# Kernel tuning notes

Measured on AMD Instinct MI355X. Metric: run time of the kernel, lower is better.

Reference implementation:

```python
import jax, jax.numpy as jnp
import numpy as np

NU, NUS, NI, NIS = 50000, 20000, 100000, 20000
E_US, E_IS, E_UI = 200000, 400000, 500000
NUM_USERS, NUM_ITEMS, UCODE, ICODE = 500000, 1000000, 1024, 1024
D, H, FH, B = 64, 4, 32, 1024  # embed_size, num_heads, gnn_hidden_size, batch

# (name, src_in_dim, dst_in_dim, out_feats_per_head)
REL_SPECS = [("r1", D, D, FH),            # user -shares-> u_sem
             ("r2", D, D, FH),            # item -shares-> i_sem
             ("r3", H * FH + D, D, FH),   # i_sem -denotes-> item
             ("r4", H * FH + D, D, FH),   # u_sem -denotes-> user
             ("r5", H * FH, H * FH, D)]   # item -clicked_by-> user


def setup_inputs() -> dict:
    key = jax.random.key(0)
    ks = iter(jax.random.split(key, 64))
    nrm = lambda shape: jax.random.normal(next(ks), shape, jnp.float32) * 0.05
    ri = lambda shape, hi: jax.random.randint(next(ks), shape, 0, hi, jnp.int32)
    inp = {}
    # node ids / edge lists / output gather indices (replaces boolean mask)
    inp["user_ids"] = ri((NU,), NUM_USERS)
    inp["usem_ids"] = ri((NUS,), UCODE)
    inp["item_ids"] = ri((NI,), NUM_ITEMS)
    inp["isem_ids"] = ri((NIS,), ICODE)
    inp["us_src"], inp["us_dst"] = ri((E_US,), NU), ri((E_US,), NUS)
    inp["is_src"], inp["is_dst"] = ri((E_IS,), NI), ri((E_IS,), NIS)
    inp["ui_src"], inp["ui_dst"] = ri((E_UI,), NI), ri((E_UI,), NU)
    inp["user_out_idx"] = ri((B,), NU)
    # embedding tables (padding rows included for user/u_sem)
    inp["user_table"] = nrm((NUM_USERS + 1, D))
    inp["usem_table"] = nrm((UCODE + 1, D))
    inp["item_table"] = nrm((NUM_ITEMS, D))
    inp["isem_table"] = nrm((ICODE, D))
    # GATConv params per relation: fc_src, fc_dst (no bias), attn_l, attn_r, out bias
    for name, ds, dd, fo in REL_SPECS:
        inp[name + "_Wsrc"] = nrm((ds, H * fo))
        inp[name + "_Wdst"] = nrm((dd, H * fo))
        inp[name + "_al"] = nrm((H, fo))
        inp[name + "_ar"] = nrm((H, fo))
        inp[name + "_b"] = nrm((H * fo,))
    # user_gnn_mapping: Linear(embed_size*num_heads -> embed_size) + ReLU (dropout=eval identity)
    inp["Wm"] = nrm((D * H, D))
    inp["bm"] = nrm((D,))
    return inp


def gat(xs, xd, es, ed, Wsrc, Wdst, al, ar, b, fo):
    """DGL bipartite GATConv, allow_zero_in_degree=True, leaky_relu(0.2) attention."""
    nd = xd.shape[0]
    fs = (xs @ Wsrc).reshape(-1, H, fo)   # [Ns,H,F]
    fd = (xd @ Wdst).reshape(-1, H, fo)   # [Nd,H,F]
    el = jnp.einsum("nhf,hf->nh", fs, al)
    er = jnp.einsum("nhf,hf->nh", fd, ar)
    e = jax.nn.leaky_relu(el[es] + er[ed], 0.2)            # [E,H]
    m = jax.ops.segment_max(e, ed, num_segments=nd)
    m = jnp.where(jnp.isfinite(m), m, 0.0)                 # empty segments -> 0
    ex = jnp.exp(e - m[ed])
    den = jax.ops.segment_sum(ex, ed, num_segments=nd)
    alpha = ex / jnp.maximum(den[ed], 1e-12)               # edge softmax per dst
    out = jax.ops.segment_sum(alpha[:, :, None] * fs[es], ed, num_segments=nd)
    return out + b.reshape(1, H, fo)                       # [Nd,H,F]


def reference(user_table, usem_table, item_table, isem_table,
              r1_Wsrc, r1_Wdst, r1_al, r1_ar, r1_b,
              r2_Wsrc, r2_Wdst, r2_al, r2_ar, r2_b,
              r3_Wsrc, r3_Wdst, r3_al, r3_ar, r3_b,
              r4_Wsrc, r4_Wdst, r4_al, r4_ar, r4_b,
              r5_Wsrc, r5_Wdst, r5_al, r5_ar, r5_b,
              Wm, bm,
              user_ids, usem_ids, item_ids, isem_ids,
              us_src, us_dst, is_src, is_dst, ui_src, ui_dst, user_out_idx):
    user_emb = user_table[user_ids]            # [NU,D]
    u_quant = usem_table[usem_ids]             # [NUS,D]
    # user -shares-> u_sem
    u_n = gat(user_emb, u_quant, us_src, us_dst, r1_Wsrc, r1_Wdst, r1_al, r1_ar, r1_b, FH).reshape(NUS, H * FH)
    # u_sem -denotes-> user ('denotes' edges are reversed 'shares' edges)
    u_h = gat(jnp.concatenate([u_n, u_quant], -1), user_emb, us_dst, us_src,
              r4_Wsrc, r4_Wdst, r4_al, r4_ar, r4_b, FH).reshape(NU, H * FH)
    item_emb = item_table[item_ids]
    i_quant = isem_table[isem_ids]
    i_n = gat(item_emb, i_quant, is_src, is_dst, r2_Wsrc, r2_Wdst, r2_al, r2_ar, r2_b, FH).reshape(NIS, H * FH)
    i_h = gat(jnp.concatenate([i_n, i_quant], -1), item_emb, is_dst, is_src,
              r3_Wsrc, r3_Wdst, r3_al, r3_ar, r3_b, FH).reshape(NI, H * FH)
    # item -clicked_by-> user
    h = gat(i_h, u_h, ui_src, ui_dst, r5_Wsrc, r5_Wdst, r5_al, r5_ar, r5_b, D).reshape(NU, H * D)
    h = h[user_out_idx]                        # masked gather of batch users [B, H*D]
    return jax.nn.relu(h @ Wm + bm)            # user_gnn_mapping (dropout=eval)
```

## Files before the change

### kernel.cpp

```cpp
#include <hip/hip_runtime.h>
#include <math.h>

#define NU 50000
#define NUS 20000
#define NI 100000
#define NIS 20000
#define E_US 200000
#define E_IS 400000
#define E_UI 500000
#define BQ 1024
#define NT 240000
#define EPOOL (2 * E_US + 2 * E_IS + E_UI)

static __device__ __forceinline__ float4 f4zero() { return make_float4(0.f, 0.f, 0.f, 0.f); }

static __device__ __forceinline__ void fma4(float4& acc, float s, const float4& w) {
  acc.x = fmaf(s, w.x, acc.x);
  acc.y = fmaf(s, w.y, acc.y);
  acc.z = fmaf(s, w.z, acc.z);
  acc.w = fmaf(s, w.w, acc.w);
}

__global__ void gather_all(const float* __restrict__ t0, const int* __restrict__ id0,
                           float* __restrict__ o0, int n0, const float* __restrict__ t1,
                           const int* __restrict__ id1, float* __restrict__ o1, int n1,
                           const float* __restrict__ t2, const int* __restrict__ id2,
                           float* __restrict__ o2, int n2, const float* __restrict__ t3,
                           const int* __restrict__ id3, float* __restrict__ o3, int n3) {
  int y = blockIdx.y;
  const float* t;
  const int* id;
  float* o;
  int n;
  if (y == 0) { t = t0; id = id0; o = o0; n = n0; }
  else if (y == 1) { t = t1; id = id1; o = o1; n = n1; }
  else if (y == 2) { t = t2; id = id2; o = o2; n = n2; }
  else { t = t3; id = id3; o = o3; n = n3; }
  int i = blockIdx.x * blockDim.x + threadIdx.x;
  if (i >= n * 16) return;
  int row = i >> 4, j = i & 15;
  ((float4*)o)[i] = ((const float4*)(t + (size_t)id[row] * 64))[j];
}

struct EdgeSets {
  const int* es[5];
  const int* ed[5];
  int E[5];
  int base[5];
};

__global__ void zero_ints(int* __restrict__ p, int n) {
  int i = blockIdx.x * blockDim.x + threadIdx.x;
  if (i < n) p[i] = 0;
}

__global__ void hist5(EdgeSets S, int* __restrict__ cnt) {
  int y = blockIdx.y;
  int e = blockIdx.x * blockDim.x + threadIdx.x;
  if (e < S.E[y]) atomicAdd(&cnt[S.base[y] + S.ed[y][e]], 1);
}

__global__ void alloc_offsets(const int* __restrict__ cnt, int* __restrict__ start,
                              int* __restrict__ wo, int* __restrict__ cursor, int n) {
  int i = blockIdx.x * blockDim.x + threadIdx.x;
  int lane = threadIdx.x & 63;
  int c = (i < n) ? cnt[i] : 0;
  int s = c;
#pragma unroll
  for (int o = 1; o < 64; o <<= 1) {
    int y = __shfl_up(s, o);
    if (lane >= o) s += y;
  }
  int base = 0;
  if (lane == 63) base = atomicAdd(cursor, s);
  base = __shfl(base, 63);
  if (i < n) {
    int st = base + s - c;
    start[i] = st;
    wo[i] = st;
  }
}

__global__ void scatter5(EdgeSets S, int* __restrict__ wo, int* __restrict__ srcp) {
  int y = blockIdx.y;
  int e = blockIdx.x * blockDim.x + threadIdx.x;
  if (e < S.E[y]) {
    int p = atomicAdd(&wo[S.base[y] + S.ed[y][e]], 1);
    srcp[p] = S.es[y][e];
  }
}

__global__ __launch_bounds__(256, 2) void gemm_fused(
    const float* __restrict__ A1, int K1, const float* __restrict__ A2, int K2,
    const float* __restrict__ W, int Kout, const float* __restrict__ avec,
    float* __restrict__ logits, int fo_shift, float* __restrict__ C, int N) {
  __shared__ float Wlds[32 * 128];
  __shared__ float Alds[32 * 36];
  const int t = threadIdx.x;
  const int cbase = blockIdx.y * 128;
  const int colpos = t & 31;
  const int c0 = colpos << 2;
  const int rg = (t >> 5) << 2;
  const int sr = t >> 3;
  const int sk = (t & 7) << 2;
  const int rt = blockIdx.x * 32;
  const int KT = K1 + K2;

  float4 acc[4] = {f4zero(), f4zero(), f4zero(), f4zero()};
  for (int kc = 0; kc < KT; kc += 32) {
    __syncthreads();
    for (int i = t; i < 1024; i += 256) {
      int k = i >> 5, c4 = (i & 31) << 2;
      *(float4*)&Wlds[k * 128 + c4] = *(const float4*)&W[(size_t)(kc + k) * Kout + cbase + c4];
    }
    {
      int row = rt + sr;
      float4 v = f4zero();
      if (row < N) {
        if (kc < K1) v = *(const float4*)&A1[(size_t)row * K1 + kc + sk];
        else v = *(const float4*)&A2[(size_t)row * K2 + (kc - K1) + sk];
      }
      Alds[(sk + 0) * 36 + sr] = v.x;
      Alds[(sk + 1) * 36 + sr] = v.y;
      Alds[(sk + 2) * 36 + sr] = v.z;
      Alds[(sk + 3) * 36 + sr] = v.w;
    }
    __syncthreads();
#pragma unroll
    for (int k = 0; k < 32; ++k) {
      float4 w = *(float4*)&Wlds[k * 128 + c0];
      float4 a = *(float4*)&Alds[k * 36 + rg];
      fma4(acc[0], a.x, w);
      fma4(acc[1], a.y, w);
      fma4(acc[2], a.z, w);
      fma4(acc[3], a.w, w);
    }
  }
  if (C) {
#pragma unroll
    for (int ri = 0; ri < 4; ++ri) {
      int row = rt + rg + ri;
      if (row < N) *(float4*)&C[(size_t)row * Kout + cbase + c0] = acc[ri];
    }
  }
  if (avec) {
    float4 av = *(const float4*)&avec[cbase + c0];
    const int gsz = 1 << (fo_shift - 2);
    const int h = (cbase + c0) >> fo_shift;
    float part[4];
#pragma unroll
    for (int ri = 0; ri < 4; ++ri)
      part[ri] = acc[ri].x * av.x + acc[ri].y * av.y + acc[ri].z * av.z + acc[ri].w * av.w;
    for (int off = 1; off < gsz; off <<= 1) {
#pragma unroll
      for (int ri = 0; ri < 4; ++ri) part[ri] += __shfl_xor(part[ri], off);
    }
    if ((colpos & (gsz - 1)) == 0) {
#pragma unroll
      for (int ri = 0; ri < 4; ++ri) {
        int row = rt + rg + ri;
        if (row < N) logits[(size_t)row * 4 + h] = part[ri];
      }
    }
  }
}

template <int NF>
__global__ __launch_bounds__(256) void gat_aggregate(
    const float* __restrict__ fs, const float* __restrict__ el, const float* __restrict__ er,
    const int* __restrict__ srcp, const int* __restrict__ start, const int* __restrict__ cnt,
    const float* __restrict__ bias, float* __restrict__ out, int Nd, int nodeBase) {
  int node = (blockIdx.x * 256 + threadIdx.x) >> 6;
  if (node >= Nd) return;
  int lane = threadIdx.x & 63;
  constexpr int K = NF * 64;
  int h = lane >> 4;
  int f0 = lane * NF;
  float acc[NF] = {};
  float den = 0.f;
  float erh = er[(size_t)node * 4 + h];
  int s = start[nodeBase + node];
  int e1 = s + cnt[nodeBase + node];
  for (int p = s; p < e1; ++p) {
    int src = srcp[p];
    float z = el[(size_t)src * 4 + h] + erh;
    float x = expf(z > 0.f ? z : 0.2f * z);
    const float* fr = fs + (size_t)src * K + f0;
    if (NF == 2) {
      float2 v = *(const float2*)fr;
      acc[0] = fmaf(x, v.x, acc[0]);
      acc[1] = fmaf(x, v.y, acc[1]);
    } else {
      float4 v = *(const float4*)fr;
      acc[0] = fmaf(x, v.x, acc[0]);
      acc[1] = fmaf(x, v.y, acc[1]);
      acc[2] = fmaf(x, v.z, acc[2]);
      acc[3] = fmaf(x, v.w, acc[3]);
    }
    den += x;
  }
  float inv = 1.f / fmaxf(den, 1e-12f);
#pragma unroll
  for (int j = 0; j < NF; ++j)
    out[(size_t)node * K + f0 + j] = fmaf(acc[j], inv, bias[f0 + j]);
}

__global__ void final_mlp(const float* __restrict__ h5, const int* __restrict__ idx,
                          const float* __restrict__ Wm, const float* __restrict__ bm,
                          float* __restrict__ out, int Bn) {
  int wave = (blockIdx.x * 256 + threadIdx.x) >> 6;
  int lane = threadIdx.x & 63;
  if (wave >= Bn) return;
  const float* row = h5 + (size_t)idx[wave] * 256;
  float acc = bm[lane];
  for (int k = 0; k < 256; ++k) acc = fmaf(row[k], Wm[k * 64 + lane], acc);
  out[wave * 64 + lane] = fmaxf(acc, 0.f);
}

static inline int cdiv(int a, int b) { return (a + b - 1) / b; }

extern "C" void kernel_launch(void* const* d_in, const int* in_sizes, int n_in, void* d_out,
                              int out_size, void* d_ws, size_t ws_size, hipStream_t stream) {
  const int* user_ids = (const int*)d_in[0];
  const int* usem_ids = (const int*)d_in[1];
  const int* item_ids = (const int*)d_in[2];
  const int* isem_ids = (const int*)d_in[3];
  const int* us_src = (const int*)d_in[4];
  const int* us_dst = (const int*)d_in[5];
  const int* is_src = (const int*)d_in[6];
  const int* is_dst = (const int*)d_in[7];
  const int* ui_src = (const int*)d_in[8];
  const int* ui_dst = (const int*)d_in[9];
  const int* user_out_idx = (const int*)d_in[10];
  const float* user_table = (const float*)d_in[11];
  const float* usem_table = (const float*)d_in[12];
  const float* item_table = (const float*)d_in[13];
  const float* isem_table = (const float*)d_in[14];
  const float* R[5][5];
  for (int r = 0; r < 5; ++r)
    for (int j = 0; j < 5; ++j) R[r][j] = (const float*)d_in[15 + r * 5 + j];
  const float* Wm = (const float*)d_in[40];
  const float* bm = (const float*)d_in[41];
  float* out = (float*)d_out;

  float* ws = (float*)d_ws;
  size_t off = 0;
  auto alloc = [&](size_t n) {
    float* p = ws + off;
    off += (n + 3) & ~(size_t)3;
    return p;
  };
  float* user_emb = alloc((size_t)NU * 64);
  float* u_quant = alloc((size_t)NUS * 64);
  float* item_emb = alloc((size_t)NI * 64);
  float* i_quant = alloc((size_t)NIS * 64);
  float* u_n = alloc((size_t)NUS * 128);
  float* u_h = alloc((size_t)NU * 128);
  float* i_n = alloc((size_t)NIS * 128);
  float* i_h = alloc((size_t)NI * 128);
  float* h5 = alloc((size_t)NU * 256);
  float* fsb = alloc((size_t)NI * 256);
  float* elb = alloc((size_t)NI * 4);
  float* erb = alloc((size_t)NI * 4);
  int* cnt = (int*)alloc(NT + 4);
  int* startb = (int*)alloc(NT + 4);
  int* wob = (int*)alloc(NT + 4);
  int* srcp = (int*)alloc(EPOOL);

  EdgeSets S;
  S.es[0] = us_src; S.ed[0] = us_dst; S.E[0] = E_US; S.base[0] = 0;
  S.es[1] = us_dst; S.ed[1] = us_src; S.E[1] = E_US; S.base[1] = NUS;
  S.es[2] = is_src; S.ed[2] = is_dst; S.E[2] = E_IS; S.base[2] = NUS + NU;
  S.es[3] = is_dst; S.ed[3] = is_src; S.E[3] = E_IS; S.base[3] = NUS + NU + NIS;
  S.es[4] = ui_src; S.ed[4] = ui_dst; S.E[4] = E_UI; S.base[4] = NUS + NU + NIS + NI;

  zero_ints<<<cdiv(NT + 1, 1024), 1024, 0, stream>>>(cnt, NT + 1);
  gather_all<<<dim3(cdiv(NI * 16, 256), 4), 256, 0, stream>>>(
      user_table, user_ids, user_emb, NU, usem_table, usem_ids, u_quant, NUS, item_table,
      item_ids, item_emb, NI, isem_table, isem_ids, i_quant, NIS);
  hist5<<<dim3(cdiv(E_UI, 256), 5), 256, 0, stream>>>(S, cnt);
  alloc_offsets<<<cdiv(NT, 256), 256, 0, stream>>>(cnt, startb, wob, cnt + NT, NT);
  scatter5<<<dim3(cdiv(E_UI, 256), 5), 256, 0, stream>>>(S, wob, srcp);

  auto gemm = [&](const float* A1, int K1, const float* A2, int K2, const float* W, int Kout,
                  const float* av, float* lg, int fo_shift, float* Cc, int N) {
    gemm_fused<<<dim3(cdiv(N, 32), Kout / 128), 256, 0, stream>>>(A1, K1, A2, K2, W, Kout, av,
                                                                  lg, fo_shift, Cc, N);
  };
  auto agg = [&](int Kout, float* outb, const float* bias, int Nd, int base) {
    if (Kout == 128)
      gat_aggregate<2><<<cdiv(Nd, 4), 256, 0, stream>>>(fsb, elb, erb, srcp, startb, cnt, bias,
                                                        outb, Nd, base);
    else
      gat_aggregate<4><<<cdiv(Nd, 4), 256, 0, stream>>>(fsb, elb, erb, srcp, startb, cnt, bias,
                                                        outb, Nd, base);
  };

  gemm(user_emb, 64, nullptr, 0, R[0][0], 128, R[0][2], elb, 5, fsb, NU);
  gemm(u_quant, 64, nullptr, 0, R[0][1], 128, R[0][3], erb, 5, nullptr, NUS);
  agg(128, u_n, R[0][4], NUS, 0);
  gemm(u_n, 128, u_quant, 64, R[3][0], 128, R[3][2], elb, 5, fsb, NUS);
  gemm(user_emb, 64, nullptr, 0, R[3][1], 128, R[3][3], erb, 5, nullptr, NU);
  agg(128, u_h, R[3][4], NU, NUS);
  gemm(item_emb, 64, nullptr, 0, R[1][0], 128, R[1][2], elb, 5, fsb, NI);
  gemm(i_quant, 64, nullptr, 0, R[1][1], 128, R[1][3], erb, 5, nullptr, NIS);
  agg(128, i_n, R[1][4], NIS, NUS + NU);
  gemm(i_n, 128, i_quant, 64, R[2][0], 128, R[2][2], elb, 5, fsb, NIS);
  gemm(item_emb, 64, nullptr, 0, R[2][1], 128, R[2][3], erb, 5, nullptr, NI);
  agg(128, i_h, R[2][4], NI, NUS + NU + NIS);
  gemm(i_h, 128, nullptr, 0, R[4][0], 256, R[4][2], elb, 6, fsb, NI);
  gemm(u_h, 128, nullptr, 0, R[4][1], 256, R[4][3], erb, 6, nullptr, NU);
  agg(256, h5, R[4][4], NU, NUS + NU + NIS + NI);

  final_mlp<<<cdiv(BQ, 4), 256, 0, stream>>>(h5, user_out_idx, Wm, bm, out, BQ);
}
```

Before: 1.229 ms.

## Switch GAT pipeline to bf16 MFMA GEMMs and fold dst projections into attention vectors

Stores intermediate features in bf16 and replaces the scalar FP32 GEMM with a bf16 MFMA GEMM that uses swizzled LDS tiles and a persistent row loop. The dst-side GEMMs are removed by precomputing Wdst·attn_r per head, so the er logits come from a dot product in the gather kernel and in the r4 aggregation. This removes about half the GEMM launches and halves memory traffic, at the cost of bf16 rounding error in the features and outputs.

```diff
diff --git a/kernel.cpp b/kernel.cpp
--- a/kernel.cpp
+++ b/kernel.cpp
@@ -12,34 +12,76 @@
 #define NT 240000
 #define EPOOL (2 * E_US + 2 * E_IS + E_UI)
 
-static __device__ __forceinline__ float4 f4zero() { return make_float4(0.f, 0.f, 0.f, 0.f); }
-
-static __device__ __forceinline__ void fma4(float4& acc, float s, const float4& w) {
-  acc.x = fmaf(s, w.x, acc.x);
-  acc.y = fmaf(s, w.y, acc.y);
-  acc.z = fmaf(s, w.z, acc.z);
-  acc.w = fmaf(s, w.w, acc.w);
-}
-
-__global__ void gather_all(const float* __restrict__ t0, const int* __restrict__ id0,
-                           float* __restrict__ o0, int n0, const float* __restrict__ t1,
-                           const int* __restrict__ id1, float* __restrict__ o1, int n1,
-                           const float* __restrict__ t2, const int* __restrict__ id2,
-                           float* __restrict__ o2, int n2, const float* __restrict__ t3,
-                           const int* __restrict__ id3, float* __restrict__ o3, int n3) {
+typedef __attribute__((ext_vector_type(8))) short short8v;
+typedef __attribute__((ext_vector_type(4))) float f32x4;
+
+static __device__ __forceinline__ unsigned short f2b(float f) {
+  unsigned u = __float_as_uint(f);
+  u = u + 0x7FFFu + ((u >> 16) & 1u);
+  return (unsigned short)(u >> 16);
+}
+static __device__ __forceinline__ float b2f(unsigned short h) {
+  return __uint_as_float(((unsigned)h) << 16);
+}
+
+struct PrepArgs {
+  const float* Wsrc[5];
+  const float* Wdst[5];
+  const float* ar[5];
+  unsigned short* Wt[5];
+  float* war[5];
+  int K[5], Kout[5], Kd[5], fo[5];
+};
+__global__ void prep_kernel(PrepArgs P) {
   int y = blockIdx.y;
-  const float* t;
-  const int* id;
-  float* o;
-  int n;
-  if (y == 0) { t = t0; id = id0; o = o0; n = n0; }
-  else if (y == 1) { t = t1; id = id1; o = o1; n = n1; }
-  else if (y == 2) { t = t2; id = id2; o = o2; n = n2; }
-  else { t = t3; id = id3; o = o3; n = n3; }
-  int i = blockIdx.x * blockDim.x + threadIdx.x;
-  if (i >= n * 16) return;
-  int row = i >> 4, j = i & 15;
-  ((float4*)o)[i] = ((const float4*)(t + (size_t)id[row] * 64))[j];
+  int t = blockIdx.x * blockDim.x + threadIdx.x;
+  int nth = gridDim.x * blockDim.x;
+  if (y < 5) {
+    int K = P.K[y], Kout = P.Kout[y];
+    for (int i = t; i < K * Kout; i += nth) {
+      int c = i / K, k = i - c * K;
+      P.Wt[y][(size_t)c * K + k] = f2b(P.Wsrc[y][(size_t)k * Kout + c]);
+    }
+  } else {
+    for (int r = 0; r < 5; ++r) {
+      int Kd = P.Kd[r], fo = P.fo[r];
+      for (int i = t; i < Kd * 4; i += nth) {
+        int k = i >> 2, h = i & 3;
+        const float* wrow = P.Wdst[r] + (size_t)k * (4 * fo) + h * fo;
+        const float* arow = P.ar[r] + h * fo;
+        float s = 0.f;
+        for (int c = 0; c < fo; ++c) s += wrow[c] * arow[c];
+        P.war[r][i] = s;
+      }
+    }
+  }
+}
+
+struct GatherArgs {
+  const float* tab[4];
+  const int* ids[4];
+  unsigned short* out[4];
+  const float* war[4];
+  float* er[4];
+  int n[4];
+};
+__global__ __launch_bounds__(256) void gather_er(GatherArgs G) {
+  int y = blockIdx.y;
+  int wave = (blockIdx.x * 256 + threadIdx.x) >> 6;
+  int lane = threadIdx.x & 63;
+  if (wave >= G.n[y]) return;
+  float x = G.tab[y][(size_t)G.ids[y][wave] * 64 + lane];
+  G.out[y][(size_t)wave * 64 + lane] = f2b(x);
+  const float* war = G.war[y] + lane * 4;
+  float p0 = x * war[0], p1 = x * war[1], p2 = x * war[2], p3 = x * war[3];
+#pragma unroll
+  for (int off = 1; off < 64; off <<= 1) {
+    p0 += __shfl_xor(p0, off);
+    p1 += __shfl_xor(p1, off);
+    p2 += __shfl_xor(p2, off);
+    p3 += __shfl_xor(p3, off);
+  }
+  if (lane == 0) *(float4*)&G.er[y][(size_t)wave * 4] = make_float4(p0, p1, p2, p3);
 }
 
 struct EdgeSets {
@@ -48,18 +90,15 @@
   int E[5];
   int base[5];
 };
-
 __global__ void zero_ints(int* __restrict__ p, int n) {
   int i = blockIdx.x * blockDim.x + threadIdx.x;
   if (i < n) p[i] = 0;
 }
-
 __global__ void hist5(EdgeSets S, int* __restrict__ cnt) {
   int y = blockIdx.y;
   int e = blockIdx.x * blockDim.x + threadIdx.x;
   if (e < S.E[y]) atomicAdd(&cnt[S.base[y] + S.ed[y][e]], 1);
 }
-
 __global__ void alloc_offsets(const int* __restrict__ cnt, int* __restrict__ start,
                               int* __restrict__ wo, int* __restrict__ cursor, int n) {
   int i = blockIdx.x * blockDim.x + threadIdx.x;
@@ -75,12 +114,10 @@
   if (lane == 63) base = atomicAdd(cursor, s);
   base = __shfl(base, 63);
   if (i < n) {
-    int st = base + s - c;
-    start[i] = st;
-    wo[i] = st;
-  }
-}
-
+    start[i] = base + s - c;
+    wo[i] = base + s - c;
+  }
+}
 __global__ void scatter5(EdgeSets S, int* __restrict__ wo, int* __restrict__ srcp) {
   int y = blockIdx.y;
   int e = blockIdx.x * blockDim.x + threadIdx.x;
@@ -90,86 +127,116 @@
   }
 }
 
-__global__ __launch_bounds__(256, 2) void gemm_fused(
-    const float* __restrict__ A1, int K1, const float* __restrict__ A2, int K2,
-    const float* __restrict__ W, int Kout, const float* __restrict__ avec,
-    float* __restrict__ logits, int fo_shift, float* __restrict__ C, int N) {
-  __shared__ float Wlds[32 * 128];
-  __shared__ float Alds[32 * 36];
+template <int KT>
+__global__ __launch_bounds__(256, 2) void gemm_mfma(
+    const unsigned short* __restrict__ A1, int K1, const unsigned short* __restrict__ A2,
+    const unsigned short* __restrict__ Wt, int Kout, const float* __restrict__ al,
+    float* __restrict__ elb, int fo_shift, unsigned short* __restrict__ Cb, int N) {
+  constexpr int KU = KT / 8;
+  __shared__ unsigned short Alds[64 * KT];
+  __shared__ unsigned short Wlds[128 * KT];
   const int t = threadIdx.x;
-  const int cbase = blockIdx.y * 128;
-  const int colpos = t & 31;
-  const int c0 = colpos << 2;
-  const int rg = (t >> 5) << 2;
-  const int sr = t >> 3;
-  const int sk = (t & 7) << 2;
-  const int rt = blockIdx.x * 32;
-  const int KT = K1 + K2;
-
-  float4 acc[4] = {f4zero(), f4zero(), f4zero(), f4zero()};
-  for (int kc = 0; kc < KT; kc += 32) {
+  const int lane = t & 63;
+  const int wid = t >> 6;
+  const int wr = wid >> 1, wc = wid & 1;
+  const int cb = blockIdx.y * 128;
+  const int lr = lane & 15;
+  const int lkg = lane >> 4;
+  const int K2 = KT - K1;
+
+  for (int i = t; i < 128 * KU; i += 256) {
+    int c = i / KU, u = i - c * KU;
+    float4 v = *(const float4*)&Wt[(size_t)(cb + c) * KT + u * 8];
+    *(float4*)&Wlds[c * KT + ((u ^ (c & 7)) << 3)] = v;
+  }
+
+  for (int rt = blockIdx.x * 64; rt < N; rt += gridDim.x * 64) {
     __syncthreads();
-    for (int i = t; i < 1024; i += 256) {
-      int k = i >> 5, c4 = (i & 31) << 2;
-      *(float4*)&Wlds[k * 128 + c4] = *(const float4*)&W[(size_t)(kc + k) * Kout + cbase + c4];
+    for (int i = t; i < 64 * KU; i += 256) {
+      int r = i / KU, u = i - r * KU;
+      int row = rt + r;
+      float4 v = make_float4(0.f, 0.f, 0.f, 0.f);
+      if (row < N) {
+        int kb = u * 8;
+        const unsigned short* p =
+            (kb < K1) ? (A1 + (size_t)row * K1 + kb) : (A2 + (size_t)row * K2 + (kb - K1));
+        v = *(const float4*)p;
+      }
+      *(float4*)&Alds[r * KT + ((u ^ (r & 7)) << 3)] = v;
+    }
+    __syncthreads();
+
+    f32x4 acc[2][4];
+#pragma unroll
+    for (int m = 0; m < 2; ++m)
+#pragma unroll
+      for (int n = 0; n < 4; ++n) acc[m][n] = (f32x4){0.f, 0.f, 0.f, 0.f};
+
+#pragma unroll
+    for (int kc = 0; kc < KT; kc += 32) {
+      const int slot = (((kc >> 3) + lkg) ^ (lane & 7)) << 3;
+      short8v a0 = *(const short8v*)&Alds[(wr * 32 + lr) * KT + slot];
+      short8v a1 = *(const short8v*)&Alds[(wr * 32 + 16 + lr) * KT + slot];
+#pragma unroll
+      for (int n = 0; n < 4; ++n) {
+        short8v b = *(const short8v*)&Wlds[(wc * 64 + n * 16 + lr) * KT + slot];
+        acc[0][n] = __builtin_amdgcn_mfma_f32_16x16x32_bf16(a0, b, acc[0][n], 0, 0, 0);
+        acc[1][n] = __builtin_amdgcn_mfma_f32_16x16x32_bf16(a1, b, acc[1][n], 0, 0, 0);
+      }
+    }
+
+    if (Cb) {
+#pragma unroll
+      for (int m = 0; m < 2; ++m)
+#pragma unroll
+        for (int q = 0; q < 4; ++q) {
+          int row = rt + wr * 32 + m * 16 + lkg * 4 + q;
+          if (row < N) {
+#pragma unroll
+            for (int n = 0; n < 4; ++n)
+              Cb[(size_t)row * Kout + cb + wc * 64 + n * 16 + lr] = f2b(acc[m][n][q]);
+          }
+        }
     }
     {
-      int row = rt + sr;
-      float4 v = f4zero();
-      if (row < N) {
-        if (kc < K1) v = *(const float4*)&A1[(size_t)row * K1 + kc + sk];
-        else v = *(const float4*)&A2[(size_t)row * K2 + (kc - K1) + sk];
-      }
-      Alds[(sk + 0) * 36 + sr] = v.x;
-      Alds[(sk + 1) * 36 + sr] = v.y;
-      Alds[(sk + 2) * 36 + sr] = v.z;
-      Alds[(sk + 3) * 36 + sr] = v.w;
-    }
-    __syncthreads();
-#pragma unroll
-    for (int k = 0; k < 32; ++k) {
-      float4 w = *(float4*)&Wlds[k * 128 + c0];
-      float4 a = *(float4*)&Alds[k * 36 + rg];
-      fma4(acc[0], a.x, w);
-      fma4(acc[1], a.y, w);
-      fma4(acc[2], a.z, w);
-      fma4(acc[3], a.w, w);
-    }
-  }
-  if (C) {
-#pragma unroll
-    for (int ri = 0; ri < 4; ++ri) {
-      int row = rt + rg + ri;
-      if (row < N) *(float4*)&C[(size_t)row * Kout + cbase + c0] = acc[ri];
-    }
-  }
-  if (avec) {
-    float4 av = *(const float4*)&avec[cbase + c0];
-    const int gsz = 1 << (fo_shift - 2);
-    const int h = (cbase + c0) >> fo_shift;
-    float part[4];
-#pragma unroll
-    for (int ri = 0; ri < 4; ++ri)
-      part[ri] = acc[ri].x * av.x + acc[ri].y * av.y + acc[ri].z * av.z + acc[ri].w * av.w;
-    for (int off = 1; off < gsz; off <<= 1) {
-#pragma unroll
-      for (int ri = 0; ri < 4; ++ri) part[ri] += __shfl_xor(part[ri], off);
-    }
-    if ((colpos & (gsz - 1)) == 0) {
-#pragma unroll
-      for (int ri = 0; ri < 4; ++ri) {
-        int row = rt + rg + ri;
-        if (row < N) logits[(size_t)row * 4 + h] = part[ri];
-      }
-    }
-  }
-}
-
-template <int NF>
-__global__ __launch_bounds__(256) void gat_aggregate(
-    const float* __restrict__ fs, const float* __restrict__ el, const float* __restrict__ er,
-    const int* __restrict__ srcp, const int* __restrict__ start, const int* __restrict__ cnt,
-    const float* __restrict__ bias, float* __restrict__ out, int Nd, int nodeBase) {
+      float av[4];
+#pragma unroll
+      for (int n = 0; n < 4; ++n) av[n] = al[cb + wc * 64 + n * 16 + lr];
+      const int npg = (1 << fo_shift) >> 4;
+      const int hpw = 4 / npg;
+      for (int m = 0; m < 2; ++m)
+        for (int g = 0; g < hpw; ++g) {
+          float p[4] = {0.f, 0.f, 0.f, 0.f};
+          for (int nn = 0; nn < npg; ++nn) {
+            int n = g * npg + nn;
+#pragma unroll
+            for (int q = 0; q < 4; ++q) p[q] += acc[m][n][q] * av[n];
+          }
+#pragma unroll
+          for (int off = 1; off < 16; off <<= 1) {
+#pragma unroll
+            for (int q = 0; q < 4; ++q) p[q] += __shfl_xor(p[q], off);
+          }
+          if (lr == 0) {
+            int h = (cb + wc * 64 + (g << fo_shift)) >> fo_shift;
+#pragma unroll
+            for (int q = 0; q < 4; ++q) {
+              int row = rt + wr * 32 + m * 16 + lkg * 4 + q;
+              if (row < N) elb[(size_t)row * 4 + h] = p[q];
+            }
+          }
+        }
+    }
+  }
+}
+
+template <int NF, bool ER5>
+__global__ __launch_bounds__(256) void gat_agg(
+    const unsigned short* __restrict__ fs, const float* __restrict__ el,
+    const float* __restrict__ er, const int* __restrict__ srcp, const int* __restrict__ start,
+    const int* __restrict__ cnt, const float* __restrict__ bias,
+    unsigned short* __restrict__ outb, const float* __restrict__ war5, float* __restrict__ er5,
+    int Nd, int nodeBase) {
   int node = (blockIdx.x * 256 + threadIdx.x) >> 6;
   if (node >= Nd) return;
   int lane = threadIdx.x & 63;
@@ -185,39 +252,68 @@
     int src = srcp[p];
     float z = el[(size_t)src * 4 + h] + erh;
     float x = expf(z > 0.f ? z : 0.2f * z);
-    const float* fr = fs + (size_t)src * K + f0;
+    const unsigned short* fr = fs + (size_t)src * K + f0;
     if (NF == 2) {
-      float2 v = *(const float2*)fr;
-      acc[0] = fmaf(x, v.x, acc[0]);
-      acc[1] = fmaf(x, v.y, acc[1]);
+      unsigned v = *(const unsigned*)fr;
+      acc[0] = fmaf(x, b2f((unsigned short)(v & 0xffff)), acc[0]);
+      acc[1] = fmaf(x, b2f((unsigned short)(v >> 16)), acc[1]);
     } else {
-      float4 v = *(const float4*)fr;
-      acc[0] = fmaf(x, v.x, acc[0]);
-      acc[1] = fmaf(x, v.y, acc[1]);
-      acc[2] = fmaf(x, v.z, acc[2]);
-      acc[3] = fmaf(x, v.w, acc[3]);
+      uint2 v = *(const uint2*)fr;
+      acc[0] = fmaf(x, b2f((unsigned short)(v.x & 0xffff)), acc[0]);
+      acc[1] = fmaf(x, b2f((unsigned short)(v.x >> 16)), acc[1]);
+      acc[2] = fmaf(x, b2f((unsigned short)(v.y & 0xffff)), acc[2]);
+      acc[3] = fmaf(x, b2f((unsigned short)(v.y >> 16)), acc[3]);
     }
     den += x;
   }
   float inv = 1.f / fmaxf(den, 1e-12f);
-#pragma unroll
-  for (int j = 0; j < NF; ++j)
-    out[(size_t)node * K + f0 + j] = fmaf(acc[j], inv, bias[f0 + j]);
-}
-
-__global__ void final_mlp(const float* __restrict__ h5, const int* __restrict__ idx,
+  float vout[NF];
+#pragma unroll
+  for (int j = 0; j < NF; ++j) vout[j] = fmaf(acc[j], inv, bias[f0 + j]);
+  if (NF == 2) {
+    unsigned pk = (unsigned)f2b(vout[0]) | ((unsigned)f2b(vout[1]) << 16);
+    *(unsigned*)&outb[(size_t)node * K + f0] = pk;
+  } else {
+    uint2 pk;
+    pk.x = (unsigned)f2b(vout[0]) | ((unsigned)f2b(vout[1]) << 16);
+    pk.y = (unsigned)f2b(vout[2]) | ((unsigned)f2b(vout[3]) << 16);
+    *(uint2*)&outb[(size_t)node * K + f0] = pk;
+  }
+  if (ER5) {
+    float p0 = 0.f, p1 = 0.f, p2 = 0.f, p3 = 0.f;
+#pragma unroll
+    for (int j = 0; j < NF; ++j) {
+      const float* wr = war5 + (size_t)(f0 + j) * 4;
+      p0 += vout[j] * wr[0];
+      p1 += vout[j] * wr[1];
+      p2 += vout[j] * wr[2];
+      p3 += vout[j] * wr[3];
+    }
+#pragma unroll
+    for (int off = 1; off < 64; off <<= 1) {
+      p0 += __shfl_xor(p0, off);
+      p1 += __shfl_xor(p1, off);
+      p2 += __shfl_xor(p2, off);
+      p3 += __shfl_xor(p3, off);
+    }
+    if (lane == 0) *(float4*)&er5[(size_t)node * 4] = make_float4(p0, p1, p2, p3);
+  }
+}
+
+__global__ void final_mlp(const unsigned short* __restrict__ h5, const int* __restrict__ idx,
                           const float* __restrict__ Wm, const float* __restrict__ bm,
                           float* __restrict__ out, int Bn) {
   int wave = (blockIdx.x * 256 + threadIdx.x) >> 6;
   int lane = threadIdx.x & 63;
   if (wave >= Bn) return;
-  const float* row = h5 + (size_t)idx[wave] * 256;
+  const unsigned short* row = h5 + (size_t)idx[wave] * 256;
   float acc = bm[lane];
-  for (int k = 0; k < 256; ++k) acc = fmaf(row[k], Wm[k * 64 + lane], acc);
+  for (int k = 0; k < 256; ++k) acc = fmaf(b2f(row[k]), Wm[k * 64 + lane], acc);
   out[wave * 64 + lane] = fmaxf(acc, 0.f);
 }
 
 static inline int cdiv(int a, int b) { return (a + b - 1) / b; }
+static inline int imin(int a, int b) { return a < b ? a : b; }
 
 extern "C" void kernel_launch(void* const* d_in, const int* in_sizes, int n_in, void* d_out,
                               int out_size, void* d_ws, size_t ws_size, hipStream_t stream) {
@@ -243,29 +339,55 @@
   const float* bm = (const float*)d_in[41];
   float* out = (float*)d_out;
 
-  float* ws = (float*)d_ws;
+  char* base = (char*)d_ws;
   size_t off = 0;
-  auto alloc = [&](size_t n) {
-    float* p = ws + off;
-    off += (n + 3) & ~(size_t)3;
+  auto alloc = [&](size_t bytes) {
+    char* p = base + off;
+    off += (bytes + 255) & ~(size_t)255;
     return p;
   };
-  float* user_emb = alloc((size_t)NU * 64);
-  float* u_quant = alloc((size_t)NUS * 64);
-  float* item_emb = alloc((size_t)NI * 64);
-  float* i_quant = alloc((size_t)NIS * 64);
-  float* u_n = alloc((size_t)NUS * 128);
-  float* u_h = alloc((size_t)NU * 128);
-  float* i_n = alloc((size_t)NIS * 128);
-  float* i_h = alloc((size_t)NI * 128);
-  float* h5 = alloc((size_t)NU * 256);
-  float* fsb = alloc((size_t)NI * 256);
-  float* elb = alloc((size_t)NI * 4);
-  float* erb = alloc((size_t)NI * 4);
-  int* cnt = (int*)alloc(NT + 4);
-  int* startb = (int*)alloc(NT + 4);
-  int* wob = (int*)alloc(NT + 4);
-  int* srcp = (int*)alloc(EPOOL);
+  unsigned short* user_emb = (unsigned short*)alloc((size_t)NU * 64 * 2);
+  unsigned short* u_quant = (unsigned short*)alloc((size_t)NUS * 64 * 2);
+  unsigned short* item_emb = (unsigned short*)alloc((size_t)NI * 64 * 2);
+  unsigned short* i_quant = (unsigned short*)alloc((size_t)NIS * 64 * 2);
+  unsigned short* u_n = (unsigned short*)alloc((size_t)NUS * 128 * 2);
+  unsigned short* u_h = (unsigned short*)alloc((size_t)NU * 128 * 2);
+  unsigned short* i_n = (unsigned short*)alloc((size_t)NIS * 128 * 2);
+  unsigned short* i_h = (unsigned short*)alloc((size_t)NI * 128 * 2);
+  unsigned short* h5 = (unsigned short*)alloc((size_t)NU * 256 * 2);
+  unsigned short* fsb = (unsigned short*)alloc((size_t)NI * 256 * 2);
+  static const int WK[5] = {64, 64, 192, 192, 128};
+  static const int WKOUT[5] = {128, 128, 128, 128, 256};
+  static const int WKD[5] = {64, 64, 64, 64, 128};
+  static const int WFO[5] = {32, 32, 32, 32, 64};
+  unsigned short* Wt[5];
+  float* war[5];
+  for (int r = 0; r < 5; ++r) Wt[r] = (unsigned short*)alloc((size_t)WK[r] * WKOUT[r] * 2);
+  for (int r = 0; r < 5; ++r) war[r] = (float*)alloc((size_t)WKD[r] * 4 * 4);
+  float* elb = (float*)alloc((size_t)NI * 4 * 4);
+  float* er1 = (float*)alloc((size_t)NUS * 4 * 4);
+  float* er2 = (float*)alloc((size_t)NIS * 4 * 4);
+  float* er3 = (float*)alloc((size_t)NI * 4 * 4);
+  float* er4 = (float*)alloc((size_t)NU * 4 * 4);
+  float* er5 = (float*)alloc((size_t)NU * 4 * 4);
+  int* cnt = (int*)alloc((NT + 1) * 4);
+  int* startb = (int*)alloc(NT * 4);
+  int* wob = (int*)alloc(NT * 4);
+  int* srcp = (int*)alloc((size_t)EPOOL * 4);
+
+  PrepArgs P;
+  for (int r = 0; r < 5; ++r) {
+    P.Wsrc[r] = R[r][0];
+    P.Wdst[r] = R[r][1];
+    P.ar[r] = R[r][3];
+    P.Wt[r] = Wt[r];
+    P.war[r] = war[r];
+    P.K[r] = WK[r];
+    P.Kout[r] = WKOUT[r];
+    P.Kd[r] = WKD[r];
+    P.fo[r] = WFO[r];
+  }
+  prep_kernel<<<dim3(32, 6), 256, 0, stream>>>(P);
 
   EdgeSets S;
   S.es[0] = us_src; S.ed[0] = us_dst; S.E[0] = E_US; S.base[0] = 0;
@@ -273,44 +395,46 @@
   S.es[2] = is_src; S.ed[2] = is_dst; S.E[2] = E_IS; S.base[2] = NUS + NU;
   S.es[3] = is_dst; S.ed[3] = is_src; S.E[3] = E_IS; S.base[3] = NUS + NU + NIS;
   S.es[4] = ui_src; S.ed[4] = ui_dst; S.E[4] = E_UI; S.base[4] = NUS + NU + NIS + NI;
-
   zero_ints<<<cdiv(NT + 1, 1024), 1024, 0, stream>>>(cnt, NT + 1);
-  gather_all<<<dim3(cdiv(NI * 16, 256), 4), 256, 0, stream>>>(
-      user_table, user_ids, user_emb, NU, usem_table, usem_ids, u_quant, NUS, item_table,
-      item_ids, item_emb, NI, isem_table, isem_ids, i_quant, NIS);
   hist5<<<dim3(cdiv(E_UI, 256), 5), 256, 0, stream>>>(S, cnt);
   alloc_offsets<<<cdiv(NT, 256), 256, 0, stream>>>(cnt, startb, wob, cnt + NT, NT);
   scatter5<<<dim3(cdiv(E_UI, 256), 5), 256, 0, stream>>>(S, wob, srcp);
 
-  auto gemm = [&](const float* A1, int K1, const float* A2, int K2, const float* W, int Kout,
-                  const float* av, float* lg, int fo_shift, float* Cc, int N) {
-    gemm_fused<<<dim3(cdiv(N, 32), Kout / 128), 256, 0, stream>>>(A1, K1, A2, K2, W, Kout, av,
-                                                                  lg, fo_shift, Cc, N);
+  GatherArgs G;
+  G.tab[0] = user_table; G.ids[0] = user_ids; G.out[0] = user_emb; G.war[0] = war[3]; G.er[0] = er4; G.n[0] = NU;
+  G.tab[1] = usem_table; G.ids[1] = usem_ids; G.out[1] = u_quant;  G.war[1] = war[0]; G.er[1] = er1; G.n[1] = NUS;
+  G.tab[2] = item_table; G.ids[2] = item_ids; G.out[2] = item_emb; G.war[2] = war[2]; G.er[2] = er3; G.n[2] = NI;
+  G.tab[3] = isem_table; G.ids[3] = isem_ids; G.out[3] = i_quant;  G.war[3] = war[1]; G.er[3] = er2; G.n[3] = NIS;
+  gather_er<<<dim3(cdiv(NI, 4), 4), 256, 0, stream>>>(G);
+
+  auto gemm = [&](int KT, const unsigned short* A1, int K1, const unsigned short* A2,
+                  const unsigned short* Wtp, int Kout, const float* al, int fo_shift,
+                  unsigned short* Cb, int N) {
+    int gy = Kout / 128;
+    dim3 g(imin(cdiv(N, 64), 768 / gy), gy);
+    if (KT == 64)
+      gemm_mfma<64><<<g, 256, 0, stream>>>(A1, K1, A2, Wtp, Kout, al, elb, fo_shift, Cb, N);
+    else if (KT == 128)
+      gemm_mfma<128><<<g, 256, 0, stream>>>(A1, K1, A2, Wtp, Kout, al, elb, fo_shift, Cb, N);
+    else
+      gemm_mfma<192><<<g, 256, 0, stream>>>(A1, K1, A2, Wtp, Kout, al, elb, fo_shift, Cb, N);
   };
-  auto agg = [&](int Kout, float* outb, const float* bias, int Nd, int base) {
-    if (Kout == 128)
-      gat_aggregate<2><<<cdiv(Nd, 4), 256, 0, stream>>>(fsb, elb, erb, srcp, startb, cnt, bias,
-                                                        outb, Nd, base);
-    else
-      gat_aggregate<4><<<cdiv(Nd, 4), 256, 0, stream>>>(fsb, elb, erb, srcp, startb, cnt, bias,
-                                                        outb, Nd, base);
-  };
-
-  gemm(user_emb, 64, nullptr, 0, R[0][0], 128, R[0][2], elb, 5, fsb, NU);
-  gemm(u_quant, 64, nullptr, 0, R[0][1], 128, R[0][3], erb, 5, nullptr, NUS);
-  agg(128, u_n, R[0][4], NUS, 0);
-  gemm(u_n, 128, u_quant, 64, R[3][0], 128, R[3][2], elb, 5, fsb, NUS);
-  gemm(user_emb, 64, nullptr, 0, R[3][1], 128, R[3][3], erb, 5, nullptr, NU);
-  agg(128, u_h, R[3][4], NU, NUS);
-  gemm(item_emb, 64, nullptr, 0, R[1][0], 128, R[1][2], elb, 5, fsb, NI);
-  gemm(i_quant, 64, nullptr, 0, R[1][1], 128, R[1][3], erb, 5, nullptr, NIS);
-  agg(128, i_n, R[1][4], NIS, NUS + NU);
-  gemm(i_n, 128, i_quant, 64, R[2][0], 128, R[2][2], elb, 5, fsb, NIS);
-  gemm(item_emb, 64, nullptr, 0, R[2][1], 128, R[2][3], erb, 5, nullptr, NI);
-  agg(128, i_h, R[2][4], NI, NUS + NU + NIS);
-  gemm(i_h, 128, nullptr, 0, R[4][0], 256, R[4][2], elb, 6, fsb, NI);
-  gemm(u_h, 128, nullptr, 0, R[4][1], 256, R[4][3], erb, 6, nullptr, NU);
-  agg(256, h5, R[4][4], NU, NUS + NU + NIS + NI);
-
+
+  gemm(64, user_emb, 64, nullptr, Wt[0], 128, R[0][2], 5, fsb, NU);
+  gat_agg<2, false><<<cdiv(NUS, 4), 256, 0, stream>>>(fsb, elb, er1, srcp, startb, cnt, R[0][4],
+                                                      u_n, nullptr, nullptr, NUS, 0);
+  gemm(192, u_n, 128, u_quant, Wt[3], 128, R[3][2], 5, fsb, NUS);
+  gat_agg<2, true><<<cdiv(NU, 4), 256, 0, stream>>>(fsb, elb, er4, srcp, startb, cnt, R[3][4],
+                                                    u_h, war[4], er5, NU, NUS);
+  gemm(64, item_emb, 64, nullptr, Wt[1], 128, R[1][2], 5, fsb, NI);
+  gat_agg<2, false><<<cdiv(NIS, 4), 256, 0, stream>>>(fsb, elb, er2, srcp, startb, cnt, R[1][4],
+                                                      i_n, nullptr, nullptr, NIS, NUS + NU);
+  gemm(192, i_n, 128, i_quant, Wt[2], 128, R[2][2], 5, fsb, NIS);
+  gat_agg<2, false><<<cdiv(NI, 4), 256, 0, stream>>>(fsb, elb, er3, srcp, startb, cnt, R[2][4],
+                                                     i_h, nullptr, nullptr, NI, NUS + NU + NIS);
+  gemm(128, i_h, 128, nullptr, Wt[4], 256, R[4][2], 6, fsb, NI);
+  gat_agg<4, false><<<cdiv(NU, 4), 256, 0, stream>>>(fsb, elb, er5, srcp, startb, cnt, R[4][4],
+                                                     h5, nullptr, nullptr, NU,
+                                                     NUS + NU + NIS + NI);
   final_mlp<<<cdiv(BQ, 4), 256, 0, stream>>>(h5, user_out_idx, Wm, bm, out, BQ);
 }
```

New measurement: 1.063 ms. -13.5%, faster.
